# Kernel tuning notes

Measured on AMD Instinct MI355X. Metric: run time of the kernel, lower is better.

## Reference

```python
import jax, jax.numpy as jnp
import numpy as np

N, SPLIT, INPUT_DIM = 16384, 100, 128
NUM_HEADS, PER_DIM = 4, 64  # out_dim = 256
NEG_SLOPE = 0.2


def setup_inputs() -> dict:
    key = jax.random.key(0)
    kx, kw, kq = jax.random.split(key, 3)
    x = jax.random.normal(kx, (N, SPLIT * INPUT_DIM), dtype=jnp.float32)
    # glorot-uniform per-head projection weights [H, input_dim, per_dim]
    limit_w = float(np.sqrt(6.0 / (INPUT_DIM + PER_DIM)))
    W = jax.random.uniform(kw, (NUM_HEADS, INPUT_DIM, PER_DIM), dtype=jnp.float32,
                           minval=-limit_w, maxval=limit_w)
    # xavier-uniform query vectors (gain=1.414) for q_ of shape [per_dim, 1] -> stored [H, per_dim]
    limit_q = float(1.414 * np.sqrt(6.0 / (PER_DIM + 1)))
    q = jax.random.uniform(kq, (NUM_HEADS, PER_DIM), dtype=jnp.float32,
                           minval=-limit_q, maxval=limit_q)
    return {"x": x, "W": W, "q": q}


def reference(x, W, q):
    n = x.shape[0]
    xs = x.reshape(n, SPLIT, INPUT_DIM)                      # [n, s, i]
    h = jnp.einsum('nsi,hio->nhso', xs, W)                   # per-head projections
    score = jax.nn.leaky_relu(jnp.einsum('nhso,ho->nhs', h, q), NEG_SLOPE)
    att = jax.nn.softmax(score, axis=2)                      # softmax over split dim
    pooled = jnp.einsum('nhso,nhs->nho', h, att)             # weighted sum pooling
    return pooled.reshape(n, NUM_HEADS * PER_DIM)            # concat heads -> [n, out_dim]
```

## Files before the change

kernel.cpp:

```cpp
#include <hip/hip_runtime.h>
#include <stdint.h>

#define NROWS 16384
#define SPLITN 100
#define IDIM 128
#define NH 4
#define PD 64
#define ROWLEN (SPLITN * IDIM)
#define ODIM (NH * PD)

typedef float f32x4 __attribute__((ext_vector_type(4)));
typedef short s16x8 __attribute__((ext_vector_type(8)));
typedef unsigned short u16x8 __attribute__((ext_vector_type(8)));

__device__ __forceinline__ unsigned short f32_to_bf16(float f) {
  uint32_t u = __float_as_uint(f);
  u += 0x7FFFu + ((u >> 16) & 1u);
  return (unsigned short)(u >> 16);
}

#if __has_builtin(__builtin_amdgcn_exp2f)
__device__ __forceinline__ float fexp2(float x) { return __builtin_amdgcn_exp2f(x); }
#else
__device__ __forceinline__ float fexp2(float x) { return exp2f(x); }
#endif

template <int IMM>
__device__ __forceinline__ float swz_f(float v) {
  return __int_as_float(__builtin_amdgcn_ds_swizzle(__float_as_int(v), IMM));
}

__global__ void prep_wq(const float* __restrict__ W, const float* __restrict__ q,
                        float* __restrict__ wq) {
  int item = blockIdx.x * 256 + threadIdx.x;
  if (item >= NH * IDIM) return;
  int h = item >> 7, i = item & (IDIM - 1);
  const float* wrow = W + (size_t)(h * IDIM + i) * PD;
  const float* qh = q + h * PD;
  float s = 0.f;
#pragma unroll 8
  for (int o = 0; o < PD; ++o) s = __builtin_fmaf(wrow[o], qh[o], s);
  wq[item] = s;
}

__global__ void prep_wp(const float* __restrict__ W, unsigned short* __restrict__ Wp) {
  int flat = blockIdx.x * 256 + threadIdx.x;
  if (flat >= 64 * 512) return;
  int f = flat >> 9;
  int rem = flat & 511;
  int l = rem >> 3, j = rem & 7;
  int of = f & 3, kb = (f >> 2) & 3, h = f >> 4;
  int k = kb * 32 + (l >> 4) * 8 + j;
  int o = of * 16 + (l & 15);
  Wp[flat] = f32_to_bf16(W[(size_t)(h * IDIM + k) * PD + o]);
}

__global__ __launch_bounds__(256) void k1(const float* __restrict__ x,
                                          const float* __restrict__ wq,
                                          unsigned short* __restrict__ ybf) {
  const int lane = threadIdx.x & 63;
  const int g = lane >> 4;
  const int li = lane & 15;
  const int row = (blockIdx.x << 2) | (threadIdx.x >> 6);
  const float* xrow = x + (size_t)row * ROWLEN;

  float wqr[NH][8];
#pragma unroll
  for (int h = 0; h < NH; ++h) {
    f32x4 a = *(const f32x4*)(wq + h * IDIM + li * 8);
    f32x4 b = *(const f32x4*)(wq + h * IDIM + li * 8 + 4);
#pragma unroll
    for (int j = 0; j < 4; ++j) { wqr[h][j] = a[j]; wqr[h][4 + j] = b[j]; }
  }

  float y[NH][8];
  float m[NH], lsum[NH], mL[NH];
#pragma unroll
  for (int h = 0; h < NH; ++h) {
    m[h] = -INFINITY; mL[h] = -INFINITY; lsum[h] = 0.f;
#pragma unroll
    for (int j = 0; j < 8; ++j) y[h][j] = 0.f;
  }
  const float L2E = 1.44269504088896340736f;

  const float* pc = xrow + g * IDIM + li * 8;
  f32x4 xa = *(const f32x4*)pc;
  f32x4 xb = *(const f32x4*)(pc + 4);

  for (int it = 0; it < 25; ++it) {
    f32x4 na = {}, nb = {};
    const float* pn = pc + 4 * IDIM;
    if (it < 24) { na = *(const f32x4*)pn; nb = *(const f32x4*)(pn + 4); }

    float xv[8];
#pragma unroll
    for (int j = 0; j < 4; ++j) { xv[j] = xa[j]; xv[4 + j] = xb[j]; }

    float part[NH];
#pragma unroll
    for (int h = 0; h < NH; ++h) {
      float p = xv[0] * wqr[h][0];
#pragma unroll
      for (int j = 1; j < 8; ++j) p = __builtin_fmaf(xv[j], wqr[h][j], p);
      part[h] = p;
    }
#pragma unroll
    for (int h = 0; h < NH; ++h) {
      part[h] += swz_f<0x041F>(part[h]);
      part[h] += swz_f<0x081F>(part[h]);
      part[h] += swz_f<0x101F>(part[h]);
      part[h] += swz_f<0x201F>(part[h]);
    }
#pragma unroll
    for (int h = 0; h < NH; ++h) {
      float sc = part[h];
      sc = sc > 0.f ? sc : 0.2f * sc;
      if (sc > m[h] + 8.0f) {
        float scale = fexp2(mL[h] - sc * L2E);
        lsum[h] *= scale;
#pragma unroll
        for (int j = 0; j < 8; ++j) y[h][j] *= scale;
        m[h] = sc; mL[h] = sc * L2E;
      }
      float w = fexp2(__builtin_fmaf(sc, L2E, -mL[h]));
      lsum[h] += w;
#pragma unroll
      for (int j = 0; j < 8; ++j) y[h][j] = __builtin_fmaf(w, xv[j], y[h][j]);
    }
    xa = na; xb = nb; pc = pn;
  }

#pragma unroll
  for (int st = 16; st <= 32; st <<= 1) {
#pragma unroll
    for (int h = 0; h < NH; ++h) {
      float mo = __shfl_xor(m[h], st, 64);
      float lo = __shfl_xor(lsum[h], st, 64);
      float mn = fmaxf(m[h], mo);
      float ea = fexp2((m[h] - mn) * L2E);
      float eb = fexp2((mo - mn) * L2E);
      lsum[h] = lsum[h] * ea + lo * eb;
#pragma unroll
      for (int j = 0; j < 8; ++j) {
        float yo = __shfl_xor(y[h][j], st, 64);
        y[h][j] = y[h][j] * ea + yo * eb;
      }
      m[h] = mn;
    }
  }

  float lg = lsum[0];
  float ys[8];
#pragma unroll
  for (int j = 0; j < 8; ++j) ys[j] = y[0][j];
#pragma unroll
  for (int h = 1; h < NH; ++h) {
    bool sel = (g == h);
    lg = sel ? lsum[h] : lg;
#pragma unroll
    for (int j = 0; j < 8; ++j) ys[j] = sel ? y[h][j] : ys[j];
  }
  float inv = 1.0f / lg;
  u16x8 pk;
#pragma unroll
  for (int j = 0; j < 8; ++j) pk[j] = f32_to_bf16(ys[j] * inv);
  *(u16x8*)(ybf + (size_t)row * 512 + g * 128 + li * 8) = pk;
}

__global__ __launch_bounds__(256) void k2(const unsigned short* ybf,
                                          const unsigned short* __restrict__ Wp,
                                          float* out) {
  const int h = threadIdx.x >> 6;
  const int l = threadIdx.x & 63;
  const int rowb = blockIdx.x * 32;

  s16x8 Bf[4][4];
#pragma unroll
  for (int kb = 0; kb < 4; ++kb)
#pragma unroll
    for (int of = 0; of < 4; ++of)
      Bf[kb][of] = *(const s16x8*)(Wp + (size_t)(((h * 4 + kb) * 4 + of) * 512 + l * 8));

  s16x8 Af[2][4];
#pragma unroll
  for (int mf = 0; mf < 2; ++mf)
#pragma unroll
    for (int kb = 0; kb < 4; ++kb) {
      int r = rowb + mf * 16 + (l & 15);
      Af[mf][kb] = *(const s16x8*)(ybf + (size_t)r * 512 + h * 128 + kb * 32 + (l >> 4) * 8);
    }

  f32x4 acc[2][4];
#pragma unroll
  for (int mf = 0; mf < 2; ++mf)
#pragma unroll
    for (int of = 0; of < 4; ++of) acc[mf][of] = (f32x4){0.f, 0.f, 0.f, 0.f};

#pragma unroll
  for (int kb = 0; kb < 4; ++kb)
#pragma unroll
    for (int mf = 0; mf < 2; ++mf)
#pragma unroll
      for (int of = 0; of < 4; ++of)
        acc[mf][of] = __builtin_amdgcn_mfma_f32_16x16x32_bf16(Af[mf][kb], Bf[kb][of],
                                                              acc[mf][of], 0, 0, 0);

#pragma unroll
  for (int mf = 0; mf < 2; ++mf)
#pragma unroll
    for (int of = 0; of < 4; ++of)
#pragma unroll
      for (int reg = 0; reg < 4; ++reg) {
        int r = rowb + mf * 16 + (l >> 4) * 4 + reg;
        int o = of * 16 + (l & 15);
        out[(size_t)r * ODIM + h * PD + o] = acc[mf][of][reg];
      }
}

extern "C" void kernel_launch(void* const* d_in, const int* in_sizes, int n_in,
                              void* d_out, int out_size, void* d_ws, size_t ws_size,
                              hipStream_t stream) {
  const float* x = (const float*)d_in[0];
  const float* W = (const float*)d_in[1];
  const float* q = (const float*)d_in[2];
  float* out = (float*)d_out;
  float* wq = (float*)d_ws;
  unsigned short* Wp = (unsigned short*)((char*)d_ws + 2048);
  unsigned short* ybf = (unsigned short*)d_out;

  prep_wq<<<2, 256, 0, stream>>>(W, q, wq);
  prep_wp<<<128, 256, 0, stream>>>(W, Wp);
  k1<<<NROWS / 4, 256, 0, stream>>>(x, wq, ybf);
  k2<<<NROWS / 32, 256, 0, stream>>>(ybf, Wp, out);
}
```

Measured before the change: 177.8 us.

## Fuse attention pooling and head projection into one kernel via shared memory

Merges the two prep kernels into one launch and fuses the pooling kernel with the MFMA projection kernel. Each 1024-thread block pools 16 rows, stages the bf16 pooled vectors in LDS, and then four waves run the bf16 MFMA projection and write the output directly. This removes the global round trip of the intermediate and two kernel launches. In exchange it uses larger blocks with a block-wide barrier, and 12 of 16 waves sit idle during the GEMM tail.

```diff
diff --git a/kernel.cpp b/kernel.cpp
--- a/kernel.cpp
+++ b/kernel.cpp
@@ -8,6 +8,7 @@
 #define PD 64
 #define ROWLEN (SPLITN * IDIM)
 #define ODIM (NH * PD)
+#define RPB 16
 
 typedef float f32x4 __attribute__((ext_vector_type(4)));
 typedef short s16x8 __attribute__((ext_vector_type(8)));
@@ -30,39 +31,42 @@
   return __int_as_float(__builtin_amdgcn_ds_swizzle(__float_as_int(v), IMM));
 }
 
-__global__ void prep_wq(const float* __restrict__ W, const float* __restrict__ q,
-                        float* __restrict__ wq) {
-  int item = blockIdx.x * 256 + threadIdx.x;
-  if (item >= NH * IDIM) return;
-  int h = item >> 7, i = item & (IDIM - 1);
-  const float* wrow = W + (size_t)(h * IDIM + i) * PD;
-  const float* qh = q + h * PD;
-  float s = 0.f;
+__global__ void prep(const float* __restrict__ W, const float* __restrict__ q,
+                     float* __restrict__ wq, unsigned short* __restrict__ Wp) {
+  if (blockIdx.x < 128) {
+    int flat = blockIdx.x * 256 + threadIdx.x;
+    int f = flat >> 9;
+    int rem = flat & 511;
+    int l = rem >> 3, j = rem & 7;
+    int of = f & 3, kb = (f >> 2) & 3, h = f >> 4;
+    int k = kb * 32 + (l >> 4) * 8 + j;
+    int o = of * 16 + (l & 15);
+    Wp[flat] = f32_to_bf16(W[(size_t)(h * IDIM + k) * PD + o]);
+  } else {
+    for (int item = threadIdx.x; item < NH * IDIM; item += 256) {
+      int h = item >> 7, i = item & (IDIM - 1);
+      const float* wrow = W + (size_t)(h * IDIM + i) * PD;
+      const float* qh = q + h * PD;
+      float s = 0.f;
 #pragma unroll 8
-  for (int o = 0; o < PD; ++o) s = __builtin_fmaf(wrow[o], qh[o], s);
-  wq[item] = s;
-}
-
-__global__ void prep_wp(const float* __restrict__ W, unsigned short* __restrict__ Wp) {
-  int flat = blockIdx.x * 256 + threadIdx.x;
-  if (flat >= 64 * 512) return;
-  int f = flat >> 9;
-  int rem = flat & 511;
-  int l = rem >> 3, j = rem & 7;
-  int of = f & 3, kb = (f >> 2) & 3, h = f >> 4;
-  int k = kb * 32 + (l >> 4) * 8 + j;
-  int o = of * 16 + (l & 15);
-  Wp[flat] = f32_to_bf16(W[(size_t)(h * IDIM + k) * PD + o]);
-}
-
-__global__ __launch_bounds__(256) void k1(const float* __restrict__ x,
-                                          const float* __restrict__ wq,
-                                          unsigned short* __restrict__ ybf) {
+      for (int o = 0; o < PD; ++o) s = __builtin_fmaf(wrow[o], qh[o], s);
+      wq[item] = s;
+    }
+  }
+}
+
+__global__ __launch_bounds__(1024) void k1(const float* __restrict__ x,
+                                           const float* __restrict__ wq,
+                                           const unsigned short* __restrict__ Wp,
+                                           float* __restrict__ out) {
+  const int w = threadIdx.x >> 6;
   const int lane = threadIdx.x & 63;
   const int g = lane >> 4;
   const int li = lane & 15;
-  const int row = (blockIdx.x << 2) | (threadIdx.x >> 6);
-  const float* xrow = x + (size_t)row * ROWLEN;
+  const int row = blockIdx.x * RPB + w;
+  const float* pc = x + (size_t)row * ROWLEN + g * IDIM + li * 8;
+
+  __shared__ unsigned short ybt[RPB][NH * IDIM + 8];
 
   float wqr[NH][8];
 #pragma unroll
@@ -83,7 +87,6 @@
   }
   const float L2E = 1.44269504088896340736f;
 
-  const float* pc = xrow + g * IDIM + li * 8;
   f32x4 xa = *(const f32x4*)pc;
   f32x4 xb = *(const f32x4*)(pc + 4);
 
@@ -122,10 +125,10 @@
         for (int j = 0; j < 8; ++j) y[h][j] *= scale;
         m[h] = sc; mL[h] = sc * L2E;
       }
-      float w = fexp2(__builtin_fmaf(sc, L2E, -mL[h]));
-      lsum[h] += w;
-#pragma unroll
-      for (int j = 0; j < 8; ++j) y[h][j] = __builtin_fmaf(w, xv[j], y[h][j]);
+      float wt = fexp2(__builtin_fmaf(sc, L2E, -mL[h]));
+      lsum[h] += wt;
+#pragma unroll
+      for (int j = 0; j < 8; ++j) y[h][j] = __builtin_fmaf(wt, xv[j], y[h][j]);
     }
     xa = na; xb = nb; pc = pn;
   }
@@ -149,72 +152,63 @@
     }
   }
 
-  float lg = lsum[0];
-  float ys[8];
-#pragma unroll
-  for (int j = 0; j < 8; ++j) ys[j] = y[0][j];
-#pragma unroll
-  for (int h = 1; h < NH; ++h) {
-    bool sel = (g == h);
-    lg = sel ? lsum[h] : lg;
-#pragma unroll
-    for (int j = 0; j < 8; ++j) ys[j] = sel ? y[h][j] : ys[j];
-  }
-  float inv = 1.0f / lg;
-  u16x8 pk;
-#pragma unroll
-  for (int j = 0; j < 8; ++j) pk[j] = f32_to_bf16(ys[j] * inv);
-  *(u16x8*)(ybf + (size_t)row * 512 + g * 128 + li * 8) = pk;
-}
-
-__global__ __launch_bounds__(256) void k2(const unsigned short* ybf,
-                                          const unsigned short* __restrict__ Wp,
-                                          float* out) {
-  const int h = threadIdx.x >> 6;
-  const int l = threadIdx.x & 63;
-  const int rowb = blockIdx.x * 32;
-
-  s16x8 Bf[4][4];
-#pragma unroll
-  for (int kb = 0; kb < 4; ++kb)
+  {
+    float lg = lsum[0];
+    float ys[8];
+#pragma unroll
+    for (int j = 0; j < 8; ++j) ys[j] = y[0][j];
+#pragma unroll
+    for (int h = 1; h < NH; ++h) {
+      bool sel = (g == h);
+      lg = sel ? lsum[h] : lg;
+#pragma unroll
+      for (int j = 0; j < 8; ++j) ys[j] = sel ? y[h][j] : ys[j];
+    }
+    float inv = 1.0f / lg;
+    u16x8 pk;
+#pragma unroll
+    for (int j = 0; j < 8; ++j) pk[j] = f32_to_bf16(ys[j] * inv);
+    *(u16x8*)&ybt[w][g * IDIM + li * 8] = pk;
+  }
+  __syncthreads();
+
+  if (w < NH) {
+    const int h = w;
+    const int l = lane;
+
+    s16x8 Bf[4][4];
+#pragma unroll
+    for (int kb = 0; kb < 4; ++kb)
+#pragma unroll
+      for (int of = 0; of < 4; ++of)
+        Bf[kb][of] = *(const s16x8*)(Wp + (size_t)(((h * 4 + kb) * 4 + of) * 512 + l * 8));
+
+    s16x8 Af[4];
+#pragma unroll
+    for (int kb = 0; kb < 4; ++kb)
+      Af[kb] = *(const s16x8*)&ybt[l & 15][h * IDIM + kb * 32 + (l >> 4) * 8];
+
+    f32x4 acc[4];
+#pragma unroll
+    for (int of = 0; of < 4; ++of) acc[of] = (f32x4){0.f, 0.f, 0.f, 0.f};
+
+#pragma unroll
+    for (int kb = 0; kb < 4; ++kb)
+#pragma unroll
+      for (int of = 0; of < 4; ++of)
+        acc[of] = __builtin_amdgcn_mfma_f32_16x16x32_bf16(Af[kb], Bf[kb][of],
+                                                          acc[of], 0, 0, 0);
+
+    const int rowb = blockIdx.x * RPB;
 #pragma unroll
     for (int of = 0; of < 4; ++of)
-      Bf[kb][of] = *(const s16x8*)(Wp + (size_t)(((h * 4 + kb) * 4 + of) * 512 + l * 8));
-
-  s16x8 Af[2][4];
-#pragma unroll
-  for (int mf = 0; mf < 2; ++mf)
-#pragma unroll
-    for (int kb = 0; kb < 4; ++kb) {
-      int r = rowb + mf * 16 + (l & 15);
-      Af[mf][kb] = *(const s16x8*)(ybf + (size_t)r * 512 + h * 128 + kb * 32 + (l >> 4) * 8);
-    }
-
-  f32x4 acc[2][4];
-#pragma unroll
-  for (int mf = 0; mf < 2; ++mf)
-#pragma unroll
-    for (int of = 0; of < 4; ++of) acc[mf][of] = (f32x4){0.f, 0.f, 0.f, 0.f};
-
-#pragma unroll
-  for (int kb = 0; kb < 4; ++kb)
-#pragma unroll
-    for (int mf = 0; mf < 2; ++mf)
-#pragma unroll
-      for (int of = 0; of < 4; ++of)
-        acc[mf][of] = __builtin_amdgcn_mfma_f32_16x16x32_bf16(Af[mf][kb], Bf[kb][of],
-                                                              acc[mf][of], 0, 0, 0);
-
-#pragma unroll
-  for (int mf = 0; mf < 2; ++mf)
-#pragma unroll
-    for (int of = 0; of < 4; ++of)
 #pragma unroll
       for (int reg = 0; reg < 4; ++reg) {
-        int r = rowb + mf * 16 + (l >> 4) * 4 + reg;
+        int r = rowb + (l >> 4) * 4 + reg;
         int o = of * 16 + (l & 15);
-        out[(size_t)r * ODIM + h * PD + o] = acc[mf][of][reg];
+        out[(size_t)r * ODIM + h * PD + o] = acc[of][reg];
       }
+  }
 }
 
 extern "C" void kernel_launch(void* const* d_in, const int* in_sizes, int n_in,
@@ -226,10 +220,7 @@
   float* out = (float*)d_out;
   float* wq = (float*)d_ws;
   unsigned short* Wp = (unsigned short*)((char*)d_ws + 2048);
-  unsigned short* ybf = (unsigned short*)d_out;
-
-  prep_wq<<<2, 256, 0, stream>>>(W, q, wq);
-  prep_wp<<<128, 256, 0, stream>>>(W, Wp);
-  k1<<<NROWS / 4, 256, 0, stream>>>(x, wq, ybf);
-  k2<<<NROWS / 32, 256, 0, stream>>>(ybf, Wp, out);
-}
+
+  prep<<<129, 256, 0, stream>>>(W, q, wq, Wp);
+  k1<<<NROWS / RPB, 1024, 0, stream>>>(x, wq, Wp, out);
+}
```

Measured after the change: 167.2 us. -6.0%, faster.
